# Optimization experiments

Hardware: AMD Instinct MI355X
Metric: run time of the kernel (lower is better)

## Reference

```python
import jax, jax.numpy as jnp
import numpy as np

N_NODES = 50000
IN_DIM = 64
OUT_DIM = 128
N_EDGES = 800000


def setup_inputs() -> dict:
    key = jax.random.key(0)
    k1, k2, k3, k4, k5 = jax.random.split(key, 5)
    x = jax.random.normal(k1, (N_NODES, IN_DIM), dtype=jnp.float32)
    edge_index = jax.random.randint(k2, (2, N_EDGES), 0, N_NODES, dtype=jnp.int64)
    # PyG SAGEConv params: lin_l (neighbor path, with bias), lin_r (root path, no bias)
    s = 1.0 / np.sqrt(IN_DIM)
    W_l = jax.random.uniform(k3, (OUT_DIM, IN_DIM), dtype=jnp.float32, minval=-s, maxval=s)
    b_l = jax.random.uniform(k4, (OUT_DIM,), dtype=jnp.float32, minval=-s, maxval=s)
    W_r = jax.random.uniform(k5, (OUT_DIM, IN_DIM), dtype=jnp.float32, minval=-s, maxval=s)
    return {"x": x, "edge_index": edge_index, "W_l": W_l, "b_l": b_l, "W_r": W_r}


def reference(x, edge_index, W_l, b_l, W_r):
    # Single-layer GraphSAGE (PyG SAGEConv, mean aggregation).
    # BasicGNN applies no activation after the last (only) layer.
    src = edge_index[0]  # message sources
    dst = edge_index[1]  # aggregation targets
    n = x.shape[0]
    # gather neighbor features and mean-aggregate per destination node
    summed = jax.ops.segment_sum(x[src], dst, num_segments=n)          # [N, IN_DIM]
    cnt = jax.ops.segment_sum(jnp.ones_like(src, dtype=x.dtype), dst, num_segments=n)
    mean = summed / jnp.clip(cnt, 1.0)[:, None]
    # out = lin_l(mean_neighbors) + lin_r(x)
    out = mean @ W_l.T + b_l + x @ W_r.T                               # [N, OUT_DIM]
    return out
```

## Files before the change

### kernel.cpp

```cpp
#include <hip/hip_runtime.h>

#define N_NODES 50000
#define IN_DIM 64
#define OUT_DIM 128
#define N_EDGES 800000

#define NPART 1024
#define EPP 782
#define NPLACE 256
#define NBUCK 512
#define NPB 98
#define WLDS 136
#define FIXSCALE 1048576.0f
#define INVFIX (1.0f / 1048576.0f)

typedef __attribute__((ext_vector_type(8))) short bf16x8;
typedef __attribute__((ext_vector_type(4))) float f32x4;

__device__ __forceinline__ unsigned short f2bf(float f) {
    unsigned u = __float_as_uint(f);
    unsigned r = u + 0x7FFFu + ((u >> 16) & 1u);
    return (unsigned short)(r >> 16);
}

__device__ __forceinline__ int SW(int nd, int f) { return (nd << 6) + (f ^ ((nd & 7) << 3)); }

__global__ __launch_bounds__(256) void p1_count_cvt(const int* __restrict__ ei,
                                                    const float* __restrict__ x,
                                                    const float* __restrict__ Wl,
                                                    const float* __restrict__ Wr,
                                                    int* __restrict__ cnt_mat,
                                                    unsigned short* __restrict__ xh,
                                                    unsigned short* __restrict__ w2h)
{
    __shared__ int h[NBUCK];
    int t = threadIdx.x, blk = blockIdx.x;
    for (int i = t; i < NBUCK; i += 256) h[i] = 0;
    __syncthreads();
    int s = blk * EPP;
    int e_end = min(s + EPP, N_EDGES);
    for (int i = s + t; i < e_end; i += 256)
        atomicAdd(&h[ei[N_EDGES + i] / NPB], 1);
    for (int gi = blk * 256 + t; gi < N_NODES * 16; gi += NPART * 256) {
        float4 v = ((const float4*)x)[gi];
        ushort4 o;
        o.x = f2bf(v.x); o.y = f2bf(v.y); o.z = f2bf(v.z); o.w = f2bf(v.w);
        ((ushort4*)xh)[gi] = o;
    }
    if (blk < 128 && t < 64) {
        w2h[blk * 128 + t]      = f2bf(Wr[blk * 64 + t]);
        w2h[blk * 128 + 64 + t] = f2bf(Wl[blk * 64 + t]);
    }
    __syncthreads();
    for (int b = t; b < NBUCK; b += 256) cnt_mat[b * NPART + blk] = h[b];
}

__global__ __launch_bounds__(256) void rowsum(const int* __restrict__ cnt_mat,
                                              int* __restrict__ tot)
{
    __shared__ int ws[4];
    int t = threadIdx.x, b = blockIdx.x;
    int lane = t & 63, w = t >> 6;
    int4 v = ((const int4*)(cnt_mat + b * NPART))[t];
    int sv = v.x + v.y + v.z + v.w;
#pragma unroll
    for (int d = 32; d >= 1; d >>= 1) sv += __shfl_down(sv, d, 64);
    if (lane == 0) ws[w] = sv;
    __syncthreads();
    if (t == 0) tot[b] = ws[0] + ws[1] + ws[2] + ws[3];
}

__global__ __launch_bounds__(256) void rowscan2(int* __restrict__ cnt_mat,
                                                const int* __restrict__ tot)
{
    __shared__ int bst_s;
    __shared__ int wtot[4];
    int t = threadIdx.x, b = blockIdx.x;
    int lane = t & 63, w = t >> 6;

    int4 mine = ((const int4*)(cnt_mat + b * NPART))[t];
    int s = mine.x + mine.y + mine.z + mine.w;
    int incl = s;
#pragma unroll
    for (int d = 1; d < 64; d <<= 1) {
        int u = __shfl_up(incl, d, 64);
        if (lane >= d) incl += u;
    }
    if (lane == 63) wtot[w] = incl;

    if (w == 0) {
        int carry = 0;
#pragma unroll
        for (int c = 0; c < 8; ++c) {
            int i = c * 64 + lane;
            int v = tot[i];
            int ic = v;
#pragma unroll
            for (int d = 1; d < 64; d <<= 1) {
                int u = __shfl_up(ic, d, 64);
                if (lane >= d) ic += u;
            }
            if (i == b) bst_s = carry + ic - v;
            carry += __shfl(ic, 63, 64);
        }
    }
    __syncthreads();
    int woff = 0;
    for (int j = 0; j < w; ++j) woff += wtot[j];
    int base = bst_s + woff + incl - s;
    int4 outv;
    outv.x = base;
    outv.y = base + mine.x;
    outv.z = base + mine.x + mine.y;
    outv.w = base + mine.x + mine.y + mine.z;
    ((int4*)(cnt_mat + b * NPART))[t] = outv;
}

__global__ __launch_bounds__(256) void bucket_place(const int* __restrict__ ei,
                                                    const int* __restrict__ cnt_scan,
                                                    unsigned* __restrict__ ebuf)
{
    __shared__ int cur[NBUCK];
    int t = threadIdx.x, blk = blockIdx.x;
    for (int b = t; b < NBUCK; b += 256) cur[b] = cnt_scan[b * NPART + blk * 4];
    __syncthreads();
    int s = blk * 4 * EPP;
    int e_end = min(s + 4 * EPP, N_EDGES);
    for (int i = s + t; i < e_end; i += 256) {
        int src = ei[i], dst = ei[N_EDGES + i];
        int bkt = dst / NPB;
        int slot = atomicAdd(&cur[bkt], 1);
        ebuf[slot] = (unsigned)src | ((unsigned)(dst - bkt * NPB) << 16);
    }
}

__global__ __launch_bounds__(1024) void gather_mfma(const unsigned short* __restrict__ xh,
                                                    const int* __restrict__ cnt_scan,
                                                    const unsigned* __restrict__ ebuf,
                                                    const unsigned short* __restrict__ w2h,
                                                    const float* __restrict__ bl,
                                                    float* __restrict__ out)
{
    __shared__ int acc[NPB * 64];
    __shared__ unsigned short wlds[128 * WLDS];
    __shared__ int dcnt[128];
    __shared__ int range_s[2];
    int t = threadIdx.x, b = blockIdx.x;
    int lane = t & 63, w = t >> 6;

#pragma unroll
    for (int c = 0; c < 2; ++c) {
        int idx = c * 1024 + t;
        int o = idx >> 4, kc = idx & 15;
        bf16x8 v = *(const bf16x8*)(w2h + o * 128 + kc * 8);
        *(bf16x8*)(&wlds[o * WLDS + kc * 8]) = v;
    }
    if (t == 0) {
        range_s[0] = cnt_scan[b * NPART];
        range_s[1] = (b < NBUCK - 1) ? cnt_scan[(b + 1) * NPART] : N_EDGES;
    }
    for (int i = t; i < NPB * 64; i += 1024) acc[i] = 0;
    if (t < 128) dcnt[t] = 0;
    __syncthreads();

    int bs = range_s[0], be = range_s[1];

    for (int e = bs + t; e < be; e += 1024)
        atomicAdd(&dcnt[(ebuf[e] >> 16) & 127], 1);

    for (int e0 = bs + w * 64; e0 < be; e0 += 1024) {
        int m = be - e0; if (m > 64) m = 64;
        unsigned pv = (lane < m) ? ebuf[e0 + lane] : 0u;
        for (int k = 0; k < m; k += 16) {
            unsigned p[16]; int fx[16];
#pragma unroll
            for (int u = 0; u < 16; ++u) p[u] = __shfl(pv, k + u, 64);
#pragma unroll
            for (int u = 0; u < 16; ++u) {
                unsigned short hv = xh[(size_t)(p[u] & 0xFFFFu) * IN_DIM + lane];
                fx[u] = __float2int_rn(__uint_as_float((unsigned)hv << 16) * FIXSCALE);
            }
#pragma unroll
            for (int u = 0; u < 16; ++u)
                if (k + u < m)
                    atomicAdd(&acc[SW((p[u] >> 16) & 127, lane)], fx[u]);
        }
    }
    __syncthreads();

    if (w < 14) {
        int strip = w >> 1, hf = w & 1;
        int row = lane & 15, q = lane >> 4;
        int in_node = strip * 16 + row;
        int in_c = (in_node < NPB) ? in_node : (NPB - 1);
        int gn = b * NPB + in_c;
        size_t nrow = (size_t)((gn < N_NODES) ? gn : (N_NODES - 1));

        bf16x8 a[4];
        a[0] = *(const bf16x8*)(xh + nrow * IN_DIM + q * 8);
        a[1] = *(const bf16x8*)(xh + nrow * IN_DIM + q * 8 + 32);

        int deg = dcnt[in_c];
        float sc = deg ? INVFIX / (float)deg : 0.0f;
        bf16x8 a2, a3;
#pragma unroll
        for (int j = 0; j < 8; ++j) {
            a2[j] = (short)f2bf((float)acc[SW(in_c, q * 8 + j)] * sc);
            a3[j] = (short)f2bf((float)acc[SW(in_c, 32 + q * 8 + j)] * sc);
        }
        a[2] = a2; a[3] = a3;

        f32x4 accf[4];
#pragma unroll
        for (int jj = 0; jj < 4; ++jj) accf[jj] = (f32x4){0.f, 0.f, 0.f, 0.f};

#pragma unroll
        for (int jj = 0; jj < 4; ++jj) {
            int ot = hf * 4 + jj;
            const unsigned short* wb = &wlds[(ot * 16 + row) * WLDS + q * 8];
#pragma unroll
            for (int s = 0; s < 4; ++s) {
                bf16x8 bfrag = *(const bf16x8*)(wb + s * 32);
                accf[jj] = __builtin_amdgcn_mfma_f32_16x16x32_bf16(a[s], bfrag, accf[jj], 0, 0, 0);
            }
        }

#pragma unroll
        for (int jj = 0; jj < 4; ++jj) {
            int ot = hf * 4 + jj;
            float bias = bl[ot * 16 + row];
#pragma unroll
            for (int r = 0; r < 4; ++r) {
                int loc = strip * 16 + q * 4 + r;
                int n = b * NPB + loc;
                if (loc < NPB && n < N_NODES)
                    out[(size_t)n * OUT_DIM + ot * 16 + row] = accf[jj][r] + bias;
            }
        }
    }
}

extern "C" void kernel_launch(void* const* d_in, const int* in_sizes, int n_in,
                              void* d_out, int out_size, void* d_ws, size_t ws_size,
                              hipStream_t stream) {
    const float* x  = (const float*)d_in[0];
    const int*   ei = (const int*)d_in[1];
    const float* Wl = (const float*)d_in[2];
    const float* bl = (const float*)d_in[3];
    const float* Wr = (const float*)d_in[4];
    float* out = (float*)d_out;

    int*            cnt_mat = (int*)d_ws;
    int*            tot     = cnt_mat + NBUCK * NPART;
    unsigned*       ebuf    = (unsigned*)(tot + NBUCK);
    unsigned short* xh      = (unsigned short*)(ebuf + N_EDGES);
    unsigned short* w2h     = xh + (size_t)N_NODES * IN_DIM;

    p1_count_cvt<<<NPART, 256, 0, stream>>>(ei, x, Wl, Wr, cnt_mat, xh, w2h);
    rowsum<<<NBUCK, 256, 0, stream>>>(cnt_mat, tot);
    rowscan2<<<NBUCK, 256, 0, stream>>>(cnt_mat, tot);
    bucket_place<<<NPLACE, 256, 0, stream>>>(ei, cnt_mat, ebuf);
    gather_mfma<<<NBUCK, 1024, 0, stream>>>(xh, cnt_mat, ebuf, w2h, bl, out);
}
```

Measured before the change: 68.77 us.

## Gather pre-quantized int16 features and load edge words as scalars

The conversion kernel now also writes an int16 fixed-point copy of x (scale 256). The gather accumulates those values straight into the LDS integer accumulators, which removes the per-element bf16-to-float-to-int conversion. Edge words are read with wave-uniform scalar loads instead of one vector load plus per-edge shuffles, and full 64-edge chunks get a fully unrolled path. The cost is an extra 6.4MB write in the first kernel and coarser quantization of x (step 1/256, with overflow risk for large values), which could hurt accuracy.

```diff
diff --git a/kernel.cpp b/kernel.cpp
--- a/kernel.cpp
+++ b/kernel.cpp
@@ -11,8 +11,8 @@
 #define NBUCK 512
 #define NPB 98
 #define WLDS 136
-#define FIXSCALE 1048576.0f
-#define INVFIX (1.0f / 1048576.0f)
+#define QSCALE 256.0f
+#define INVQ (1.0f / 256.0f)
 
 typedef __attribute__((ext_vector_type(8))) short bf16x8;
 typedef __attribute__((ext_vector_type(4))) float f32x4;
@@ -31,6 +31,7 @@
                                                     const float* __restrict__ Wr,
                                                     int* __restrict__ cnt_mat,
                                                     unsigned short* __restrict__ xh,
+                                                    short* __restrict__ xq,
                                                     unsigned short* __restrict__ w2h)
 {
     __shared__ int h[NBUCK];
@@ -46,6 +47,12 @@
         ushort4 o;
         o.x = f2bf(v.x); o.y = f2bf(v.y); o.z = f2bf(v.z); o.w = f2bf(v.w);
         ((ushort4*)xh)[gi] = o;
+        short4 q;
+        q.x = (short)__float2int_rn(v.x * QSCALE);
+        q.y = (short)__float2int_rn(v.y * QSCALE);
+        q.z = (short)__float2int_rn(v.z * QSCALE);
+        q.w = (short)__float2int_rn(v.w * QSCALE);
+        ((short4*)xq)[gi] = q;
     }
     if (blk < 128 && t < 64) {
         w2h[blk * 128 + t]      = f2bf(Wr[blk * 64 + t]);
@@ -135,6 +142,7 @@
 }
 
 __global__ __launch_bounds__(1024) void gather_mfma(const unsigned short* __restrict__ xh,
+                                                    const short* __restrict__ xq,
                                                     const int* __restrict__ cnt_scan,
                                                     const unsigned* __restrict__ ebuf,
                                                     const unsigned short* __restrict__ w2h,
@@ -163,27 +171,41 @@
     if (t < 128) dcnt[t] = 0;
     __syncthreads();
 
-    int bs = range_s[0], be = range_s[1];
+    int bs = __builtin_amdgcn_readfirstlane(range_s[0]);
+    int be = __builtin_amdgcn_readfirstlane(range_s[1]);
 
     for (int e = bs + t; e < be; e += 1024)
         atomicAdd(&dcnt[(ebuf[e] >> 16) & 127], 1);
 
-    for (int e0 = bs + w * 64; e0 < be; e0 += 1024) {
+    int wu = __builtin_amdgcn_readfirstlane(w);
+    for (int e0 = bs + wu * 64; e0 < be; e0 += 1024) {
         int m = be - e0; if (m > 64) m = 64;
-        unsigned pv = (lane < m) ? ebuf[e0 + lane] : 0u;
-        for (int k = 0; k < m; k += 16) {
-            unsigned p[16]; int fx[16];
-#pragma unroll
-            for (int u = 0; u < 16; ++u) p[u] = __shfl(pv, k + u, 64);
-#pragma unroll
-            for (int u = 0; u < 16; ++u) {
-                unsigned short hv = xh[(size_t)(p[u] & 0xFFFFu) * IN_DIM + lane];
-                fx[u] = __float2int_rn(__uint_as_float((unsigned)hv << 16) * FIXSCALE);
-            }
-#pragma unroll
-            for (int u = 0; u < 16; ++u)
-                if (k + u < m)
-                    atomicAdd(&acc[SW((p[u] >> 16) & 127, lane)], fx[u]);
+        if (m == 64) {
+#pragma unroll
+            for (int k = 0; k < 64; k += 16) {
+                unsigned p[16];
+#pragma unroll
+                for (int u = 0; u < 16; ++u) p[u] = ebuf[e0 + k + u];
+                int hv[16];
+#pragma unroll
+                for (int u = 0; u < 16; ++u) {
+                    int src = (int)(p[u] & 0xFFFFu);
+                    hv[u] = (int)xq[src * IN_DIM + lane];
+                }
+                int sa[16];
+#pragma unroll
+                for (int u = 0; u < 16; ++u)
+                    sa[u] = SW((int)((p[u] >> 16) & 127u), lane);
+#pragma unroll
+                for (int u = 0; u < 16; ++u) atomicAdd(&acc[sa[u]], hv[u]);
+            }
+        } else {
+            for (int k = 0; k < m; ++k) {
+                unsigned p = ebuf[e0 + k];
+                int src = (int)(p & 0xFFFFu);
+                int hv = (int)xq[src * IN_DIM + lane];
+                atomicAdd(&acc[SW((int)((p >> 16) & 127u), lane)], hv);
+            }
         }
     }
     __syncthreads();
@@ -201,7 +223,7 @@
         a[1] = *(const bf16x8*)(xh + nrow * IN_DIM + q * 8 + 32);
 
         int deg = dcnt[in_c];
-        float sc = deg ? INVFIX / (float)deg : 0.0f;
+        float sc = deg ? INVQ / (float)deg : 0.0f;
         bf16x8 a2, a3;
 #pragma unroll
         for (int j = 0; j < 8; ++j) {
@@ -254,11 +276,12 @@
     int*            tot     = cnt_mat + NBUCK * NPART;
     unsigned*       ebuf    = (unsigned*)(tot + NBUCK);
     unsigned short* xh      = (unsigned short*)(ebuf + N_EDGES);
-    unsigned short* w2h     = xh + (size_t)N_NODES * IN_DIM;
-
-    p1_count_cvt<<<NPART, 256, 0, stream>>>(ei, x, Wl, Wr, cnt_mat, xh, w2h);
+    short*          xq      = (short*)(xh + (size_t)N_NODES * IN_DIM);
+    unsigned short* w2h     = (unsigned short*)(xq + (size_t)N_NODES * IN_DIM);
+
+    p1_count_cvt<<<NPART, 256, 0, stream>>>(ei, x, Wl, Wr, cnt_mat, xh, xq, w2h);
     rowsum<<<NBUCK, 256, 0, stream>>>(cnt_mat, tot);
     rowscan2<<<NBUCK, 256, 0, stream>>>(cnt_mat, tot);
     bucket_place<<<NPLACE, 256, 0, stream>>>(ei, cnt_mat, ebuf);
-    gather_mfma<<<NBUCK, 1024, 0, stream>>>(xh, cnt_mat, ebuf, w2h, bl, out);
-}
+    gather_mfma<<<NBUCK, 1024, 0, stream>>>(xh, xq, cnt_mat, ebuf, w2h, bl, out);
+}
```

Measured after the change: 67.75 us. No clear change (-1.5%).
